# Optimization experiments

Hardware: AMD Instinct MI355X
Metric: run time of the kernel (lower is better)

## Reference

```python
import jax, jax.numpy as jnp
import numpy as np

PAGE_SIZE = 16
HQ, HKV, D = 32, 8, 128   # num_q_heads, num_kv_heads, head_dim
B, S = 8, 1024            # requests, tokens per request (prefill)


def setup_inputs() -> dict:
    key = jax.random.key(0)
    ks = jax.random.split(key, 4)
    T = B * S
    q = jax.random.normal(ks[0], (T, HQ * D), jnp.float32)
    k = jax.random.normal(ks[1], (T, HKV * D), jnp.float32)
    v = jax.random.normal(ks[2], (T, HKV * D), jnp.float32)
    pages_per_seq = S // PAGE_SIZE          # 64
    num_pages = B * pages_per_seq + 64      # 576 (with slack pages)
    # random page assignment: each request owns pages_per_seq distinct pages
    perm = jax.random.permutation(ks[3], num_pages)[: B * pages_per_seq]
    page_table = perm.reshape(B, pages_per_seq).astype(jnp.int32)
    key_buf = jnp.zeros((num_pages * PAGE_SIZE, HKV, D), jnp.float32)
    value_buf = jnp.zeros((num_pages * PAGE_SIZE, HKV, D), jnp.float32)
    return {"q": q, "k": k, "v": v, "key_buf": key_buf,
            "value_buf": value_buf, "page_table": page_table}


def reference(q, k, v, key_buf, value_buf, page_table):
    Bq, P = page_table.shape
    S_ = P * PAGE_SIZE
    T = Bq * S_
    scale = 1.0 / np.sqrt(D).astype(np.float32)

    k3 = k.reshape(T, HKV, D)
    v3 = v.reshape(T, HKV, D)

    # store_kv_cache: scatter new tokens into the paged KV buffers
    # token (b, s) -> slot page_table[b, s//PAGE_SIZE]*PAGE_SIZE + s%PAGE_SIZE
    slots = (page_table[:, :, None] * PAGE_SIZE
             + jnp.arange(PAGE_SIZE, dtype=page_table.dtype)).reshape(-1)  # [T]
    kb = key_buf.at[slots].set(k3)
    vb = value_buf.at[slots].set(v3)

    # prefill attention: gather each request's KV from the paged cache
    K = kb[slots].reshape(Bq, S_, HKV, D)
    V = vb[slots].reshape(Bq, S_, HKV, D)
    Q = q.reshape(Bq, S_, HKV, HQ // HKV, D)  # GQA grouping: g = HQ//HKV

    scores = jnp.einsum('bqhgd,bkhd->bhgqk', Q, K) * scale  # [B,Hkv,g,S,S]
    causal = jnp.tril(jnp.ones((S_, S_), dtype=bool))
    scores = jnp.where(causal, scores, jnp.float32(-1e30))
    p = jax.nn.softmax(scores, axis=-1)
    out = jnp.einsum('bhgqk,bkhd->bqhgd', p, V)  # [B,S,Hkv,g,D]
    return out.reshape(T, HQ * D)
```

## Files before the change

kernel.cpp:

```cpp
#include <hip/hip_runtime.h>

typedef _Float16 f16;
typedef __attribute__((ext_vector_type(8))) _Float16 f16x8;
typedef __attribute__((ext_vector_type(4))) _Float16 f16x4;
typedef __attribute__((ext_vector_type(4))) float f32x4;

constexpr int HQ = 32, HKV = 8, D = 128, NB = 8, S = 1024;
constexpr float SCALE_LOG2E = 0.08838834764831845f * 1.4426950408889634f;

__global__ __launch_bounds__(256) void kpack_kernel(const float* __restrict__ k,
                                                    f16* __restrict__ kf) {
    int c = blockIdx.x * 256 + threadIdx.x;
    int lane = c & 63;
    int kb = (c >> 6) & 3, mb = (c >> 8) & 3, tile = (c >> 10) & 15;
    int hk = (c >> 14) & 7, b = (c >> 17);
    int quad = lane >> 4, lq = lane & 15;
    int s = tile * 64 + mb * 16 + lq;
    int d = kb * 32 + quad * 8;
    const float* src = k + ((size_t)(b * S + s) * HKV + hk) * D + d;
    float4 x = *(const float4*)src;
    float4 y = *(const float4*)(src + 4);
    f16x8 o = { (f16)x.x,(f16)x.y,(f16)x.z,(f16)x.w,
                (f16)y.x,(f16)y.y,(f16)y.z,(f16)y.w };
    *(f16x8*)(kf + (size_t)c * 8) = o;
}

__global__ __launch_bounds__(256) void vpack_kernel(const float* __restrict__ v,
                                                    f16* __restrict__ vf) {
    int c = blockIdx.x * 256 + threadIdx.x;
    int lane = c & 63;
    int ks2 = (c >> 6) & 1, mi = (c >> 7) & 7, tile = (c >> 10) & 15;
    int hk = (c >> 14) & 7, b = (c >> 17);
    int quad = lane >> 4, lq = lane & 15;
    int d = mi * 16 + lq;
    f16 buf[8];
#pragma unroll
    for (int o = 0; o < 2; o++)
#pragma unroll
        for (int j = 0; j < 4; j++) {
            int s = tile * 64 + ks2 * 32 + o * 16 + quad * 4 + j;
            buf[o * 4 + j] = (f16)v[((size_t)(b * S + s) * HKV + hk) * D + d];
        }
    *(f16x8*)(vf + (size_t)c * 8) = *(const f16x8*)buf;
}

__global__ __launch_bounds__(256, 3) void attn_kernel(
    const float* __restrict__ q, const f16* __restrict__ kf,
    const f16* __restrict__ vf, float* __restrict__ out) {

    int id = blockIdx.x;
    int qt = 7 - (id >> 8);
    int r = id & 255;
    int b = r >> 5, hq = r & 31, hk = hq >> 2;

    int t = threadIdx.x;
    int w = t >> 6, lane = t & 63, quad = lane >> 4, lq = lane & 15;
    int qwb = qt * 128 + w * 32;

    f16x8 qf[2][4];
#pragma unroll
    for (int nq = 0; nq < 2; nq++) {
        int qg = qwb + nq * 16 + lq;
        const float* qp = q + ((size_t)(b * S + qg) * HQ + hq) * D + quad * 8;
#pragma unroll
        for (int kb = 0; kb < 4; kb++) {
            float4 x = *(const float4*)(qp + kb * 32);
            float4 y = *(const float4*)(qp + kb * 32 + 4);
            qf[nq][kb] = (f16x8){ (f16)x.x,(f16)x.y,(f16)x.z,(f16)x.w,
                                  (f16)y.x,(f16)y.y,(f16)y.z,(f16)y.w };
        }
    }

    f32x4 zero4 = { 0.f, 0.f, 0.f, 0.f };
    f32x4 oacc[8][2];
#pragma unroll
    for (int mi = 0; mi < 8; mi++) { oacc[mi][0] = zero4; oacc[mi][1] = zero4; }
    float m_i[2] = { -1e30f, -1e30f };
    float l_i[2] = { 0.f, 0.f };

    const f16* kfb = kf + (size_t)(b * 8 + hk) * (S * D);
    const f16* vfb = vf + (size_t)(b * 8 + hk) * (S * D);

    int nt = qwb / 64 + 1;

    for (int kt = 0; kt < nt; kt++) {
        f32x4 sacc[4][2];
#pragma unroll
        for (int mb = 0; mb < 4; mb++) { sacc[mb][0] = zero4; sacc[mb][1] = zero4; }
#pragma unroll
        for (int mb = 0; mb < 4; mb++) {
            const f16* ka = kfb + (size_t)(((kt * 4 + mb) * 4) * 64 + lane) * 8;
#pragma unroll
            for (int kb = 0; kb < 4; kb++) {
                f16x8 af = *(const f16x8*)(ka + kb * 512);
                sacc[mb][0] = __builtin_amdgcn_mfma_f32_16x16x32_f16(af, qf[0][kb], sacc[mb][0], 0, 0, 0);
                sacc[mb][1] = __builtin_amdgcn_mfma_f32_16x16x32_f16(af, qf[1][kb], sacc[mb][1], 0, 0, 0);
            }
        }

        bool diag = (kt == nt - 1);
        f16x4 pf[4][2];
#pragma unroll
        for (int nq = 0; nq < 2; nq++) {
            float mt = -1e30f;
            if (diag) {
                int qg = qwb + nq * 16 + lq;
#pragma unroll
                for (int mb = 0; mb < 4; mb++)
#pragma unroll
                    for (int r4 = 0; r4 < 4; r4++) {
                        float vs = sacc[mb][nq][r4] * SCALE_LOG2E;
                        int key = kt * 64 + mb * 16 + quad * 4 + r4;
                        vs = (key <= qg) ? vs : -1e30f;
                        sacc[mb][nq][r4] = vs;
                        mt = fmaxf(mt, vs);
                    }
            } else {
#pragma unroll
                for (int mb = 0; mb < 4; mb++)
#pragma unroll
                    for (int r4 = 0; r4 < 4; r4++) {
                        float vs = sacc[mb][nq][r4] * SCALE_LOG2E;
                        sacc[mb][nq][r4] = vs;
                        mt = fmaxf(mt, vs);
                    }
            }
            mt = fmaxf(mt, __shfl_xor(mt, 16, 64));
            mt = fmaxf(mt, __shfl_xor(mt, 32, 64));
            float mnew = fmaxf(m_i[nq], mt);
            float a = exp2f(m_i[nq] - mnew);
            m_i[nq] = mnew;
            float ls = 0.f;
#pragma unroll
            for (int mb = 0; mb < 4; mb++)
#pragma unroll
                for (int r4 = 0; r4 < 4; r4++) {
                    float e = exp2f(sacc[mb][nq][r4] - mnew);
                    sacc[mb][nq][r4] = e;
                    ls += e;
                }
            ls += __shfl_xor(ls, 16, 64);
            ls += __shfl_xor(ls, 32, 64);
            l_i[nq] = l_i[nq] * a + ls;
#pragma unroll
            for (int mb = 0; mb < 4; mb++)
                pf[mb][nq] = (f16x4){ (f16)sacc[mb][nq][0], (f16)sacc[mb][nq][1],
                                      (f16)sacc[mb][nq][2], (f16)sacc[mb][nq][3] };
#pragma unroll
            for (int mi = 0; mi < 8; mi++) oacc[mi][nq] = oacc[mi][nq] * a;
        }

#pragma unroll
        for (int mi = 0; mi < 8; mi++) {
            const f16* va = vfb + (size_t)(((kt * 8 + mi) * 2) * 64 + lane) * 8;
#pragma unroll
            for (int ks2 = 0; ks2 < 2; ks2++) {
                f16x8 vv = *(const f16x8*)(va + ks2 * 512);
                f16x4 v0 = { vv[0], vv[1], vv[2], vv[3] };
                f16x4 v1 = { vv[4], vv[5], vv[6], vv[7] };
                oacc[mi][0] = __builtin_amdgcn_mfma_f32_16x16x16f16(v0, pf[ks2 * 2 + 0][0], oacc[mi][0], 0, 0, 0);
                oacc[mi][0] = __builtin_amdgcn_mfma_f32_16x16x16f16(v1, pf[ks2 * 2 + 1][0], oacc[mi][0], 0, 0, 0);
                oacc[mi][1] = __builtin_amdgcn_mfma_f32_16x16x16f16(v0, pf[ks2 * 2 + 0][1], oacc[mi][1], 0, 0, 0);
                oacc[mi][1] = __builtin_amdgcn_mfma_f32_16x16x16f16(v1, pf[ks2 * 2 + 1][1], oacc[mi][1], 0, 0, 0);
            }
        }
    }

#pragma unroll
    for (int nq = 0; nq < 2; nq++) {
        float linv = 1.0f / l_i[nq];
        int qg = qwb + nq * 16 + lq;
        float* op = out + ((size_t)(b * S + qg) * HQ + hq) * D + quad * 4;
#pragma unroll
        for (int mi = 0; mi < 8; mi++) {
            float4 vv = { oacc[mi][nq][0] * linv, oacc[mi][nq][1] * linv,
                          oacc[mi][nq][2] * linv, oacc[mi][nq][3] * linv };
            *(float4*)(op + mi * 16) = vv;
        }
    }
}

extern "C" void kernel_launch(void* const* d_in, const int* in_sizes, int n_in,
                              void* d_out, int out_size, void* d_ws, size_t ws_size,
                              hipStream_t stream) {
    (void)in_sizes; (void)n_in; (void)out_size; (void)ws_size;
    const float* q = (const float*)d_in[0];
    const float* k = (const float*)d_in[1];
    const float* v = (const float*)d_in[2];
    float* out = (float*)d_out;

    f16* kf = (f16*)d_ws;
    f16* vf = kf + (size_t)NB * HKV * S * D;

    kpack_kernel<<<4096, 256, 0, stream>>>(k, kf);
    vpack_kernel<<<4096, 256, 0, stream>>>(v, vf);
    attn_kernel<<<NB * HQ * 8, 256, 0, stream>>>(q, kf, vf, out);
}
```

Before: 491.8 us.

## Coalesce K packing, XCD-aware block mapping, lazy rescale, and MFMA priority hints

The K pack kernel is reorganised so each block reads contiguous rows of K and scatters them into the packed layout, which coalesces the global reads. The attention grid is remapped so blocks that share a batch and KV head land on the same XCD, which should improve L2 reuse of packed K/V. The softmax scale is folded into Q at load time, and the running max is only updated when it grows by more than 8 in log2 units, which skips most exp and accumulator rescaling. The kernel also converts P with packed round-toward-zero conversion and raises wave priority around the MFMA blocks. The lazy max update lets exponents reach up to 2^8 before a rescale, and fp16 rounding changes slightly, so accuracy and overflow headroom need checking.

```diff
diff --git a/kernel.cpp b/kernel.cpp
--- a/kernel.cpp
+++ b/kernel.cpp
@@ -10,19 +10,21 @@
 
 __global__ __launch_bounds__(256) void kpack_kernel(const float* __restrict__ k,
                                                     f16* __restrict__ kf) {
-    int c = blockIdx.x * 256 + threadIdx.x;
-    int lane = c & 63;
-    int kb = (c >> 6) & 3, mb = (c >> 8) & 3, tile = (c >> 10) & 15;
-    int hk = (c >> 14) & 7, b = (c >> 17);
-    int quad = lane >> 4, lq = lane & 15;
-    int s = tile * 64 + mb * 16 + lq;
-    int d = kb * 32 + quad * 8;
-    const float* src = k + ((size_t)(b * S + s) * HKV + hk) * D + d;
+    int blk = blockIdx.x;
+    int mb = blk & 3, tile = (blk >> 2) & 15, hk = (blk >> 6) & 7, b = blk >> 9;
+    int t = threadIdx.x;
+    int s_local = t >> 4;
+    int dg = t & 15;
+    int s = tile * 64 + mb * 16 + s_local;
+    const float* src = k + ((size_t)(b * S + s) * HKV + hk) * D + dg * 8;
     float4 x = *(const float4*)src;
     float4 y = *(const float4*)(src + 4);
     f16x8 o = { (f16)x.x,(f16)x.y,(f16)x.z,(f16)x.w,
                 (f16)y.x,(f16)y.y,(f16)y.z,(f16)y.w };
-    *(f16x8*)(kf + (size_t)c * 8) = o;
+    int kb = dg >> 2, quad = dg & 3;
+    size_t c = ((((size_t)(b * 8 + hk) * 16 + tile) * 4 + mb) * 4 + kb) * 64
+             + quad * 16 + s_local;
+    *(f16x8*)(kf + c * 8) = o;
 }
 
 __global__ __launch_bounds__(256) void vpack_kernel(const float* __restrict__ v,
@@ -49,9 +51,14 @@
     const f16* __restrict__ vf, float* __restrict__ out) {
 
     int id = blockIdx.x;
-    int qt = 7 - (id >> 8);
-    int r = id & 255;
-    int b = r >> 5, hq = r & 31, hk = hq >> 2;
+    int xcd = id & 7;
+    int slot = id >> 3;
+    int gl = slot >> 5;
+    int inner = slot & 31;
+    int g = gl * 8 + xcd;
+    int b = g >> 3, hk = g & 7;
+    int hq = (hk << 2) | (inner & 3);
+    int qt = 7 - (inner >> 2);
 
     int t = threadIdx.x;
     int w = t >> 6, lane = t & 63, quad = lane >> 4, lq = lane & 15;
@@ -66,8 +73,11 @@
         for (int kb = 0; kb < 4; kb++) {
             float4 x = *(const float4*)(qp + kb * 32);
             float4 y = *(const float4*)(qp + kb * 32 + 4);
-            qf[nq][kb] = (f16x8){ (f16)x.x,(f16)x.y,(f16)x.z,(f16)x.w,
-                                  (f16)y.x,(f16)y.y,(f16)y.z,(f16)y.w };
+            qf[nq][kb] = (f16x8){
+                (f16)(x.x * SCALE_LOG2E), (f16)(x.y * SCALE_LOG2E),
+                (f16)(x.z * SCALE_LOG2E), (f16)(x.w * SCALE_LOG2E),
+                (f16)(y.x * SCALE_LOG2E), (f16)(y.y * SCALE_LOG2E),
+                (f16)(y.z * SCALE_LOG2E), (f16)(y.w * SCALE_LOG2E) };
         }
     }
 
@@ -87,6 +97,7 @@
         f32x4 sacc[4][2];
 #pragma unroll
         for (int mb = 0; mb < 4; mb++) { sacc[mb][0] = zero4; sacc[mb][1] = zero4; }
+        __builtin_amdgcn_s_setprio(1);
 #pragma unroll
         for (int mb = 0; mb < 4; mb++) {
             const f16* ka = kfb + (size_t)(((kt * 4 + mb) * 4) * 64 + lane) * 8;
@@ -97,6 +108,7 @@
                 sacc[mb][1] = __builtin_amdgcn_mfma_f32_16x16x32_f16(af, qf[1][kb], sacc[mb][1], 0, 0, 0);
             }
         }
+        __builtin_amdgcn_s_setprio(0);
 
         bool diag = (kt == nt - 1);
         f16x4 pf[4][2];
@@ -109,7 +121,7 @@
                 for (int mb = 0; mb < 4; mb++)
 #pragma unroll
                     for (int r4 = 0; r4 < 4; r4++) {
-                        float vs = sacc[mb][nq][r4] * SCALE_LOG2E;
+                        float vs = sacc[mb][nq][r4];
                         int key = kt * 64 + mb * 16 + quad * 4 + r4;
                         vs = (key <= qg) ? vs : -1e30f;
                         sacc[mb][nq][r4] = vs;
@@ -119,37 +131,39 @@
 #pragma unroll
                 for (int mb = 0; mb < 4; mb++)
 #pragma unroll
-                    for (int r4 = 0; r4 < 4; r4++) {
-                        float vs = sacc[mb][nq][r4] * SCALE_LOG2E;
-                        sacc[mb][nq][r4] = vs;
-                        mt = fmaxf(mt, vs);
-                    }
+                    for (int r4 = 0; r4 < 4; r4++)
+                        mt = fmaxf(mt, sacc[mb][nq][r4]);
             }
             mt = fmaxf(mt, __shfl_xor(mt, 16, 64));
             mt = fmaxf(mt, __shfl_xor(mt, 32, 64));
-            float mnew = fmaxf(m_i[nq], mt);
-            float a = exp2f(m_i[nq] - mnew);
-            m_i[nq] = mnew;
+            float mnew = m_i[nq];
+            if (!__all(mt <= mnew + 8.0f)) {
+                mnew = fmaxf(mnew, mt);
+                float a = exp2f(m_i[nq] - mnew);
+                m_i[nq] = mnew;
+                l_i[nq] *= a;
+#pragma unroll
+                for (int mi = 0; mi < 8; mi++) oacc[mi][nq] = oacc[mi][nq] * a;
+            }
             float ls = 0.f;
 #pragma unroll
-            for (int mb = 0; mb < 4; mb++)
+            for (int mb = 0; mb < 4; mb++) {
 #pragma unroll
                 for (int r4 = 0; r4 < 4; r4++) {
                     float e = exp2f(sacc[mb][nq][r4] - mnew);
                     sacc[mb][nq][r4] = e;
                     ls += e;
                 }
+                auto lo = __builtin_amdgcn_cvt_pkrtz(sacc[mb][nq][0], sacc[mb][nq][1]);
+                auto hi = __builtin_amdgcn_cvt_pkrtz(sacc[mb][nq][2], sacc[mb][nq][3]);
+                pf[mb][nq] = (f16x4){ (f16)lo[0], (f16)lo[1], (f16)hi[0], (f16)hi[1] };
+            }
             ls += __shfl_xor(ls, 16, 64);
             ls += __shfl_xor(ls, 32, 64);
-            l_i[nq] = l_i[nq] * a + ls;
-#pragma unroll
-            for (int mb = 0; mb < 4; mb++)
-                pf[mb][nq] = (f16x4){ (f16)sacc[mb][nq][0], (f16)sacc[mb][nq][1],
-                                      (f16)sacc[mb][nq][2], (f16)sacc[mb][nq][3] };
-#pragma unroll
-            for (int mi = 0; mi < 8; mi++) oacc[mi][nq] = oacc[mi][nq] * a;
-        }
-
+            l_i[nq] += ls;
+        }
+
+        __builtin_amdgcn_s_setprio(1);
 #pragma unroll
         for (int mi = 0; mi < 8; mi++) {
             const f16* va = vfb + (size_t)(((kt * 8 + mi) * 2) * 64 + lane) * 8;
@@ -164,6 +178,7 @@
                 oacc[mi][1] = __builtin_amdgcn_mfma_f32_16x16x16f16(v1, pf[ks2 * 2 + 1][1], oacc[mi][1], 0, 0, 0);
             }
         }
+        __builtin_amdgcn_s_setprio(0);
     }
 
 #pragma unroll
```

Result: no change. 485.4 us (-1.3%).
